# Performance work log

Hardware: AMD Instinct MI355X
Metric: run time of the kernel (lower is better)

The kernel has to match this reference:

```python
import jax, jax.numpy as jnp
import numpy as np

N, M, D = 8192, 8192, 1024

def setup_inputs() -> dict:
    key = jax.random.key(0)
    k1, k2 = jax.random.split(key)
    encoder_outputs = jax.random.normal(k1, (N, D), dtype=jnp.float32)
    fact_emb = jax.random.normal(k2, (M, D), dtype=jnp.float32)
    return {"encoder_outputs": encoder_outputs, "fact_emb": fact_emb}

def reference(encoder_outputs, fact_emb):
    # energy: [N, M] = encoder_outputs @ fact_emb^T (unscaled)
    energy = jnp.einsum('nd,md->nm', encoder_outputs, fact_emb)
    weights = jax.nn.softmax(energy, axis=1)          # softmax over facts
    outputs = jnp.einsum('nm,md->nd', weights, fact_emb)
    return (outputs, weights)
```

## Files before the change

kernel.cpp:

```cpp
#include <hip/hip_runtime.h>
#include <hip/hip_bf16.h>
#include <math.h>
#include <stdint.h>

#define N_ROWS 8192
#define M_FACTS 8192
#define D_DIM 1024

typedef __bf16 bf16x8_t __attribute__((ext_vector_type(8)));
typedef __bf16 bf16x4_t __attribute__((ext_vector_type(4)));
typedef float f32x4_t __attribute__((ext_vector_type(4)));

#define BM 128
#define BN 128
#define BK 32
#define PADK 40

__device__ __forceinline__ void gload_lds16(const void* g, void* lds) {
  __builtin_amdgcn_global_load_lds(
      (__attribute__((address_space(1))) void*)(uintptr_t)g,
      (__attribute__((address_space(3))) void*)(uint32_t)(uintptr_t)lds,
      16, 0, 0);
}

#define WAIT_VMCNT(n) __builtin_amdgcn_s_waitcnt(0x0F70 | (n))


__global__ __launch_bounds__(256) void split_hi_lo(const float* __restrict__ X,
                                                   __bf16* __restrict__ H,
                                                   __bf16* __restrict__ L) {
  int i = blockIdx.x * 256 + threadIdx.x;
  float4 v = ((const float4*)X)[i];
  float f[4] = {v.x, v.y, v.z, v.w};
  bf16x4_t h, l;
#pragma unroll
  for (int q = 0; q < 4; q++) {
    __bf16 hh = (__bf16)f[q];
    h[q] = hh;
    l[q] = (__bf16)(f[q] - (float)hh);
  }
  ((bf16x4_t*)H)[i] = h;
  ((bf16x4_t*)L)[i] = l;
}

__global__ __launch_bounds__(256) void transpose_f_bf16(const float* __restrict__ F,
                                                        __bf16* __restrict__ Ft) {
  __shared__ __bf16 t[64 * 68];
  const int tid = threadIdx.x;
  const int m0 = blockIdx.x * 64, d0 = blockIdx.y * 64;
#pragma unroll
  for (int p = 0; p < 4; p++) {
    int flat = p * 256 + tid;
    int m = flat >> 4, dq = flat & 15;
    float4 v = *(const float4*)(F + (size_t)(m0 + m) * D_DIM + d0 + dq * 4);
    bf16x4_t h;
    h[0] = (__bf16)v.x;
    h[1] = (__bf16)v.y;
    h[2] = (__bf16)v.z;
    h[3] = (__bf16)v.w;
    *(bf16x4_t*)(t + m * 68 + dq * 4) = h;
  }
  __syncthreads();
  int d = tid & 63, mc = (tid >> 6) * 16;
  bf16x8_t o0, o1;
#pragma unroll
  for (int j = 0; j < 8; j++) o0[j] = t[(mc + j) * 68 + d];
#pragma unroll
  for (int j = 0; j < 8; j++) o1[j] = t[(mc + 8 + j) * 68 + d];
  __bf16* dst = Ft + (size_t)(d0 + d) * M_FACTS + m0 + mc;
  *(bf16x8_t*)(dst) = o0;
  *(bf16x8_t*)(dst + 8) = o1;
}

__global__ __launch_bounds__(256) void gemm1_fast(const __bf16* __restrict__ Eh,
                                                  const __bf16* __restrict__ El,
                                                  const __bf16* __restrict__ Fh,
                                                  const __bf16* __restrict__ Fl,
                                                  float* __restrict__ C) {
  __shared__ __bf16 sAh[BM * BK], sAl[BM * BK], sBh[BN * BK], sBl[BN * BK];
  const int tid = threadIdx.x;
  const int wave = tid >> 6, lane = tid & 63;
  const int row0 = blockIdx.x * BM, col0 = blockIdx.y * BN;
  const int wm = wave >> 1, wn = wave & 1;
  const int lrow = lane & 15, quad = lane >> 4;

  f32x4_t acc[4][4];
#pragma unroll
  for (int i = 0; i < 4; i++)
#pragma unroll
    for (int j = 0; j < 4; j++) acc[i][j] = (f32x4_t){0.f, 0.f, 0.f, 0.f};

  for (int k0 = 0; k0 < D_DIM; k0 += BK) {
#pragma unroll
    for (int r = 0; r < 2; r++) {
      int c = (r * 4 + wave) * 64 + lane;
      int row = c >> 2;
      int ko = (c & 3) << 3;
      size_t ga = (size_t)(row0 + row) * D_DIM + k0 + ko;
      size_t gb = (size_t)(col0 + row) * D_DIM + k0 + ko;
      gload_lds16(Eh + ga, sAh + c * 8);
      gload_lds16(El + ga, sAl + c * 8);
      gload_lds16(Fh + gb, sBh + c * 8);
      gload_lds16(Fl + gb, sBl + c * 8);
    }
    __syncthreads();

    bf16x8_t ah[4], al[4], bh[4], bl[4];
#pragma unroll
    for (int i = 0; i < 4; i++) {
      int ra = (wm * 64 + i * 16 + lrow) * BK + quad * 8;
      ah[i] = *(const bf16x8_t*)(sAh + ra);
      al[i] = *(const bf16x8_t*)(sAl + ra);
      int rb = (wn * 64 + i * 16 + lrow) * BK + quad * 8;
      bh[i] = *(const bf16x8_t*)(sBh + rb);
      bl[i] = *(const bf16x8_t*)(sBl + rb);
    }
#pragma unroll
    for (int i = 0; i < 4; i++)
#pragma unroll
      for (int j = 0; j < 4; j++) {
        acc[i][j] = __builtin_amdgcn_mfma_f32_16x16x32_bf16(ah[i], bh[j], acc[i][j], 0, 0, 0);
        acc[i][j] = __builtin_amdgcn_mfma_f32_16x16x32_bf16(ah[i], bl[j], acc[i][j], 0, 0, 0);
        acc[i][j] = __builtin_amdgcn_mfma_f32_16x16x32_bf16(al[i], bh[j], acc[i][j], 0, 0, 0);
      }
    __syncthreads();
  }

#pragma unroll
  for (int i = 0; i < 4; i++) {
    int rbase = row0 + wm * 64 + i * 16 + quad * 4;
#pragma unroll
    for (int j = 0; j < 4; j++) {
      int c = col0 + wn * 64 + j * 16 + lrow;
#pragma unroll
      for (int r = 0; r < 4; r++) C[(size_t)(rbase + r) * M_FACTS + c] = acc[i][j][r];
    }
  }
}

#define G2BK 64
__global__ __launch_bounds__(256) void gemm2_db(const __bf16* __restrict__ Wb,
                                                const __bf16* __restrict__ Ft,
                                                float* __restrict__ O,
                                                int out_row0) {
  __shared__ __bf16 sW[2][BM * G2BK];
  __shared__ __bf16 sF[2][BN * G2BK];
  const int tid = threadIdx.x;
  const int wave = tid >> 6, lane = tid & 63;
  const int col0 = blockIdx.x * BN;
  const int row0 = blockIdx.y * BM;
  const int wm = wave >> 1, wn = wave & 1;
  const int lrow = lane & 15, quad = lane >> 4;

  const int lr = lane >> 3;
  const int lk = (lane & 7) * 8;

  f32x4_t acc[4][4];
#pragma unroll
  for (int i = 0; i < 4; i++)
#pragma unroll
    for (int j = 0; j < 4; j++) acc[i][j] = (f32x4_t){0.f, 0.f, 0.f, 0.f};

#pragma unroll
  for (int r = 0; r < 4; r++) {
    int c = wave * 4 + r;
    int row = c * 8 + lr;
    gload_lds16(Wb + (size_t)(row0 + row) * M_FACTS + 0 + lk, &sW[0][c * 512 + lane * 8]);
    gload_lds16(Ft + (size_t)(col0 + row) * M_FACTS + 0 + lk, &sF[0][c * 512 + lane * 8]);
  }

  int buf = 0;
  for (int k0 = 0; k0 < M_FACTS; k0 += G2BK) {
    const bool more = (k0 + G2BK) < M_FACTS;
    if (more) {
      int nb = buf ^ 1;
#pragma unroll
      for (int r = 0; r < 4; r++) {
        int c = wave * 4 + r;
        int row = c * 8 + lr;
        gload_lds16(Wb + (size_t)(row0 + row) * M_FACTS + (k0 + G2BK) + lk,
                    &sW[nb][c * 512 + lane * 8]);
        gload_lds16(Ft + (size_t)(col0 + row) * M_FACTS + (k0 + G2BK) + lk,
                    &sF[nb][c * 512 + lane * 8]);
      }
      WAIT_VMCNT(8);
    } else {
      WAIT_VMCNT(0);
    }
    __builtin_amdgcn_s_barrier();

#pragma unroll
    for (int ks = 0; ks < G2BK; ks += 32) {
      bf16x8_t a[4], b[4];
#pragma unroll
      for (int i = 0; i < 4; i++) {
        a[i] = *(const bf16x8_t*)(&sW[buf][(wm * 64 + i * 16 + lrow) * G2BK + ks + quad * 8]);
        b[i] = *(const bf16x8_t*)(&sF[buf][(wn * 64 + i * 16 + lrow) * G2BK + ks + quad * 8]);
      }
#pragma unroll
      for (int i = 0; i < 4; i++)
#pragma unroll
        for (int j = 0; j < 4; j++)
          acc[i][j] = __builtin_amdgcn_mfma_f32_16x16x32_bf16(a[i], b[j], acc[i][j], 0, 0, 0);
    }
    __builtin_amdgcn_s_barrier();
    buf ^= 1;
  }

#pragma unroll
  for (int i = 0; i < 4; i++) {
    int rbase = out_row0 + row0 + wm * 64 + i * 16 + quad * 4;
#pragma unroll
    for (int j = 0; j < 4; j++) {
      int c = col0 + wn * 64 + j * 16 + lrow;
#pragma unroll
      for (int r = 0; r < 4; r++) O[(size_t)(rbase + r) * D_DIM + c] = acc[i][j][r];
    }
  }
}

__global__ __launch_bounds__(256) void gemm2_mid(const float* __restrict__ W,
                                                 const __bf16* __restrict__ Ft,
                                                 float* __restrict__ O) {
  __shared__ __bf16 sW[BM * BK], sF[BN * BK];
  const int tid = threadIdx.x;
  const int wave = tid >> 6, lane = tid & 63;
  const int row0 = blockIdx.x * BM, col0 = blockIdx.y * BN;
  const int wm = wave >> 1, wn = wave & 1;
  const int lrow = lane & 15, quad = lane >> 4;

  f32x4_t acc[4][4];
#pragma unroll
  for (int i = 0; i < 4; i++)
#pragma unroll
    for (int j = 0; j < 4; j++) acc[i][j] = (f32x4_t){0.f, 0.f, 0.f, 0.f};

  for (int k0 = 0; k0 < M_FACTS; k0 += BK) {
#pragma unroll
    for (int r = 0; r < 2; r++) {
      int c = (r * 4 + wave) * 64 + lane;
      int row = c >> 2;
      int ko = (c & 3) << 3;
      gload_lds16(Ft + (size_t)(col0 + row) * M_FACTS + k0 + ko, sF + c * 8);
    }
#pragma unroll
    for (int it = 0; it < 4; it++) {
      int flat = it * 256 + tid;
      int r = flat >> 3, q = flat & 7;
      float4 v = *(const float4*)(W + (size_t)(row0 + r) * M_FACTS + k0 + q * 4);
      bf16x4_t h;
      h[0] = (__bf16)v.x;
      h[1] = (__bf16)v.y;
      h[2] = (__bf16)v.z;
      h[3] = (__bf16)v.w;
      *(bf16x4_t*)(sW + r * BK + q * 4) = h;
    }
    __syncthreads();

    bf16x8_t a[4], b[4];
#pragma unroll
    for (int i = 0; i < 4; i++) {
      a[i] = *(const bf16x8_t*)(sW + (wm * 64 + i * 16 + lrow) * BK + quad * 8);
      b[i] = *(const bf16x8_t*)(sF + (wn * 64 + i * 16 + lrow) * BK + quad * 8);
    }
#pragma unroll
    for (int i = 0; i < 4; i++)
#pragma unroll
      for (int j = 0; j < 4; j++)
        acc[i][j] = __builtin_amdgcn_mfma_f32_16x16x32_bf16(a[i], b[j], acc[i][j], 0, 0, 0);
    __syncthreads();
  }

#pragma unroll
  for (int i = 0; i < 4; i++) {
    int rbase = row0 + wm * 64 + i * 16 + quad * 4;
#pragma unroll
    for (int j = 0; j < 4; j++) {
      int c = col0 + wn * 64 + j * 16 + lrow;
#pragma unroll
      for (int r = 0; r < 4; r++) O[(size_t)(rbase + r) * D_DIM + c] = acc[i][j][r];
    }
  }
}

template <bool EMIT_BF16>
__global__ __launch_bounds__(256) void softmax_rows_t(float* __restrict__ W,
                                                      __bf16* __restrict__ Wb) {
  __shared__ float red[8];
  const int tid = threadIdx.x;
  float* p = W + (size_t)blockIdx.x * M_FACTS;

  float4 v[8];
  float mx = -3.4e38f;
#pragma unroll
  for (int i = 0; i < 8; i++) {
    v[i] = *(const float4*)(p + (size_t)(i * 256 + tid) * 4);
    mx = fmaxf(mx, fmaxf(fmaxf(v[i].x, v[i].y), fmaxf(v[i].z, v[i].w)));
  }
#pragma unroll
  for (int off = 32; off >= 1; off >>= 1) mx = fmaxf(mx, __shfl_xor(mx, off));
  const int wave = tid >> 6, lane = tid & 63;
  if (lane == 0) red[wave] = mx;
  __syncthreads();
  mx = fmaxf(fmaxf(red[0], red[1]), fmaxf(red[2], red[3]));

  float s = 0.f;
#pragma unroll
  for (int i = 0; i < 8; i++) {
    v[i].x = __expf(v[i].x - mx);
    v[i].y = __expf(v[i].y - mx);
    v[i].z = __expf(v[i].z - mx);
    v[i].w = __expf(v[i].w - mx);
    s += v[i].x + v[i].y + v[i].z + v[i].w;
  }
#pragma unroll
  for (int off = 32; off >= 1; off >>= 1) s += __shfl_xor(s, off);
  if (lane == 0) red[4 + wave] = s;
  __syncthreads();
  s = red[4] + red[5] + red[6] + red[7];
  float inv = 1.0f / s;
  __bf16* pb = EMIT_BF16 ? (Wb + (size_t)blockIdx.x * M_FACTS) : nullptr;
#pragma unroll
  for (int i = 0; i < 8; i++) {
    v[i].x *= inv;
    v[i].y *= inv;
    v[i].z *= inv;
    v[i].w *= inv;
    *(float4*)(p + (size_t)(i * 256 + tid) * 4) = v[i];
    if (EMIT_BF16) {
      bf16x4_t h;
      h[0] = (__bf16)v[i].x;
      h[1] = (__bf16)v[i].y;
      h[2] = (__bf16)v[i].z;
      h[3] = (__bf16)v[i].w;
      *(bf16x4_t*)(pb + (size_t)(i * 256 + tid) * 4) = h;
    }
  }
}

__global__ __launch_bounds__(256) void gemm1_energy(const float* __restrict__ A,
                                                    const float* __restrict__ B,
                                                    float* __restrict__ C) {
  __shared__ __align__(16) __bf16 sAh[BM * PADK];
  __shared__ __align__(16) __bf16 sAl[BM * PADK];
  __shared__ __align__(16) __bf16 sBh[BN * PADK];
  __shared__ __align__(16) __bf16 sBl[BN * PADK];

  const int tid = threadIdx.x;
  const int row0 = blockIdx.x * BM, col0 = blockIdx.y * BN;
  const int wave = tid >> 6, lane = tid & 63;
  const int wm = wave >> 1, wn = wave & 1;
  const int lrow = lane & 15, quad = lane >> 4;

  f32x4_t acc[4][4];
#pragma unroll
  for (int i = 0; i < 4; i++)
#pragma unroll
    for (int j = 0; j < 4; j++) acc[i][j] = (f32x4_t){0.f, 0.f, 0.f, 0.f};

  for (int k0 = 0; k0 < D_DIM; k0 += BK) {
    __syncthreads();
#pragma unroll
    for (int it = 0; it < 4; it++) {
      int flat = it * 256 + tid;
      int r = flat >> 3, kq = flat & 7;
      float4 va = *(const float4*)(A + (size_t)(row0 + r) * D_DIM + k0 + kq * 4);
      float4 vb = *(const float4*)(B + (size_t)(col0 + r) * D_DIM + k0 + kq * 4);
      float fa[4] = {va.x, va.y, va.z, va.w};
      float fb[4] = {vb.x, vb.y, vb.z, vb.w};
      bf16x4_t ah, al, bh, bl;
#pragma unroll
      for (int q = 0; q < 4; q++) {
        __bf16 h = (__bf16)fa[q];
        ah[q] = h;
        al[q] = (__bf16)(fa[q] - (float)h);
        __bf16 g = (__bf16)fb[q];
        bh[q] = g;
        bl[q] = (__bf16)(fb[q] - (float)g);
      }
      *(bf16x4_t*)(sAh + r * PADK + kq * 4) = ah;
      *(bf16x4_t*)(sAl + r * PADK + kq * 4) = al;
      *(bf16x4_t*)(sBh + r * PADK + kq * 4) = bh;
      *(bf16x4_t*)(sBl + r * PADK + kq * 4) = bl;
    }
    __syncthreads();

    bf16x8_t a_h[4], a_l[4], b_h[4], b_l[4];
#pragma unroll
    for (int i = 0; i < 4; i++) {
      int ra = wm * 64 + i * 16 + lrow;
      a_h[i] = *(const bf16x8_t*)(sAh + ra * PADK + quad * 8);
      a_l[i] = *(const bf16x8_t*)(sAl + ra * PADK + quad * 8);
      int rb = wn * 64 + i * 16 + lrow;
      b_h[i] = *(const bf16x8_t*)(sBh + rb * PADK + quad * 8);
      b_l[i] = *(const bf16x8_t*)(sBl + rb * PADK + quad * 8);
    }
#pragma unroll
    for (int i = 0; i < 4; i++)
#pragma unroll
      for (int j = 0; j < 4; j++) {
        acc[i][j] = __builtin_amdgcn_mfma_f32_16x16x32_bf16(a_h[i], b_h[j], acc[i][j], 0, 0, 0);
        acc[i][j] = __builtin_amdgcn_mfma_f32_16x16x32_bf16(a_h[i], b_l[j], acc[i][j], 0, 0, 0);
        acc[i][j] = __builtin_amdgcn_mfma_f32_16x16x32_bf16(a_l[i], b_h[j], acc[i][j], 0, 0, 0);
      }
  }

#pragma unroll
  for (int i = 0; i < 4; i++) {
    int rbase = row0 + wm * 64 + i * 16 + quad * 4;
#pragma unroll
    for (int j = 0; j < 4; j++) {
      int c = col0 + wn * 64 + j * 16 + lrow;
#pragma unroll
      for (int r = 0; r < 4; r++) C[(size_t)(rbase + r) * M_FACTS + c] = acc[i][j][r];
    }
  }
}

__global__ __launch_bounds__(256) void gemm2_out(const float* __restrict__ W,
                                                 const float* __restrict__ F,
                                                 float* __restrict__ O) {
  __shared__ __align__(16) __bf16 sW[BM * PADK];
  __shared__ __align__(16) __bf16 sFt[BN * PADK];

  const int tid = threadIdx.x;
  const int row0 = blockIdx.x * BM, col0 = blockIdx.y * BN;
  const int wave = tid >> 6, lane = tid & 63;
  const int wm = wave >> 1, wn = wave & 1;
  const int lrow = lane & 15, quad = lane >> 4;

  f32x4_t acc[4][4];
#pragma unroll
  for (int i = 0; i < 4; i++)
#pragma unroll
    for (int j = 0; j < 4; j++) acc[i][j] = (f32x4_t){0.f, 0.f, 0.f, 0.f};

  for (int k0 = 0; k0 < M_FACTS; k0 += BK) {
    __syncthreads();
#pragma unroll
    for (int it = 0; it < 4; it++) {
      int flat = it * 256 + tid;
      int r = flat >> 3, kq = flat & 7;
      float4 v = *(const float4*)(W + (size_t)(row0 + r) * M_FACTS + k0 + kq * 4);
      bf16x4_t h;
      h[0] = (__bf16)v.x;
      h[1] = (__bf16)v.y;
      h[2] = (__bf16)v.z;
      h[3] = (__bf16)v.w;
      *(bf16x4_t*)(sW + r * PADK + kq * 4) = h;
    }
#pragma unroll
    for (int it = 0; it < 4; it++) {
      int flat = it * 256 + tid;
      int m = flat >> 5, dq = flat & 31;
      float4 v = *(const float4*)(F + (size_t)(k0 + m) * D_DIM + col0 + dq * 4);
      sFt[(dq * 4 + 0) * PADK + m] = (__bf16)v.x;
      sFt[(dq * 4 + 1) * PADK + m] = (__bf16)v.y;
      sFt[(dq * 4 + 2) * PADK + m] = (__bf16)v.z;
      sFt[(dq * 4 + 3) * PADK + m] = (__bf16)v.w;
    }
    __syncthreads();

    bf16x8_t a[4], b[4];
#pragma unroll
    for (int i = 0; i < 4; i++) {
      a[i] = *(const bf16x8_t*)(sW + (wm * 64 + i * 16 + lrow) * PADK + quad * 8);
      b[i] = *(const bf16x8_t*)(sFt + (wn * 64 + i * 16 + lrow) * PADK + quad * 8);
    }
#pragma unroll
    for (int i = 0; i < 4; i++)
#pragma unroll
      for (int j = 0; j < 4; j++)
        acc[i][j] = __builtin_amdgcn_mfma_f32_16x16x32_bf16(a[i], b[j], acc[i][j], 0, 0, 0);
  }

#pragma unroll
  for (int i = 0; i < 4; i++) {
    int rbase = row0 + wm * 64 + i * 16 + quad * 4;
#pragma unroll
    for (int j = 0; j < 4; j++) {
      int c = col0 + wn * 64 + j * 16 + lrow;
#pragma unroll
      for (int r = 0; r < 4; r++) O[(size_t)(rbase + r) * D_DIM + c] = acc[i][j][r];
    }
  }
}

extern "C" void kernel_launch(void* const* d_in, const int* in_sizes, int n_in,
                              void* d_out, int out_size, void* d_ws, size_t ws_size,
                              hipStream_t stream) {
  const float* E = (const float*)d_in[0];
  const float* F = (const float*)d_in[1];
  float* outputs = (float*)d_out;
  float* weights = (float*)d_out + (size_t)N_ROWS * D_DIM;

  const size_t MB = 1ull << 20;
  char* ws = (char*)d_ws;

  const bool t1 = ws_size >= 144 * MB;
  const bool t2 = !t1 && ws_size >= 80 * MB;
  const bool hasFtOnly = !t1 && !t2 && ws_size >= 16 * MB;

  if (t1 || t2) {
    __bf16* Ft = (__bf16*)(ws + 0 * MB);
    __bf16* Eh = (__bf16*)(ws + 16 * MB);
    __bf16* El = (__bf16*)(ws + 32 * MB);
    __bf16* Fh = (__bf16*)(ws + 48 * MB);
    __bf16* Fl = (__bf16*)(ws + 64 * MB);
    __bf16* Wb = (__bf16*)(ws + 16 * MB);

    transpose_f_bf16<<<dim3(M_FACTS / 64, D_DIM / 64), 256, 0, stream>>>(F, Ft);
    split_hi_lo<<<dim3((N_ROWS * D_DIM) / 1024), 256, 0, stream>>>(E, Eh, El);
    split_hi_lo<<<dim3((M_FACTS * D_DIM) / 1024), 256, 0, stream>>>(F, Fh, Fl);
    gemm1_fast<<<dim3(N_ROWS / BM, M_FACTS / BN), 256, 0, stream>>>(Eh, El, Fh, Fl, weights);

    if (t1) {
      softmax_rows_t<true><<<dim3(N_ROWS), 256, 0, stream>>>(weights, Wb);
      gemm2_db<<<dim3(D_DIM / BN, N_ROWS / BM), 256, 0, stream>>>(Wb, Ft, outputs, 0);
    } else {
      const int HALF = N_ROWS / 2;
      for (int h = 0; h < 2; h++) {
        float* Wchunk = weights + (size_t)h * HALF * M_FACTS;
        softmax_rows_t<true><<<dim3(HALF), 256, 0, stream>>>(Wchunk, Wb);
        gemm2_db<<<dim3(D_DIM / BN, HALF / BM), 256, 0, stream>>>(Wb, Ft, outputs, h * HALF);
      }
    }
  } else {
    __bf16* Ft = (__bf16*)ws;
    if (hasFtOnly) {
      transpose_f_bf16<<<dim3(M_FACTS / 64, D_DIM / 64), 256, 0, stream>>>(F, Ft);
    }
    gemm1_energy<<<dim3(N_ROWS / BM, M_FACTS / BN), 256, 0, stream>>>(E, F, weights);
    softmax_rows_t<false><<<dim3(N_ROWS), 256, 0, stream>>>(weights, nullptr);
    if (hasFtOnly) {
      gemm2_mid<<<dim3(N_ROWS / BM, D_DIM / BN), 256, 0, stream>>>(weights, Ft, outputs);
    } else {
      gemm2_out<<<dim3(N_ROWS / BM, D_DIM / BN), 256, 0, stream>>>(weights, F, outputs);
    }
  }
}
```

Baseline: 998.8 us.

## Register-staged gemm2 pipeline, chunked gemm1 launches, fp32 LDS transpose

Replaces the async global-to-LDS double-buffered gemm2 with a version that prefetches the next K tile into registers and then writes it into a double-buffered LDS tile, using a smaller K step. gemm1 is split into eight launches over row bands, presumably for better L2 reuse of the F operand. The transpose kernel now stages fp32 values transposed in LDS and converts to bf16 on the way out. The aim is better latency hiding and cache locality, at the cost of more launches and extra register and LDS store traffic.

```diff
diff --git a/kernel.cpp b/kernel.cpp
--- a/kernel.cpp
+++ b/kernel.cpp
@@ -22,8 +22,6 @@
       (__attribute__((address_space(3))) void*)(uint32_t)(uintptr_t)lds,
       16, 0, 0);
 }
-
-#define WAIT_VMCNT(n) __builtin_amdgcn_s_waitcnt(0x0F70 | (n))
 
 
 __global__ __launch_bounds__(256) void split_hi_lo(const float* __restrict__ X,
@@ -45,7 +43,7 @@
 
 __global__ __launch_bounds__(256) void transpose_f_bf16(const float* __restrict__ F,
                                                         __bf16* __restrict__ Ft) {
-  __shared__ __bf16 t[64 * 68];
+  __shared__ float t[64 * 69];
   const int tid = threadIdx.x;
   const int m0 = blockIdx.x * 64, d0 = blockIdx.y * 64;
 #pragma unroll
@@ -53,34 +51,34 @@
     int flat = p * 256 + tid;
     int m = flat >> 4, dq = flat & 15;
     float4 v = *(const float4*)(F + (size_t)(m0 + m) * D_DIM + d0 + dq * 4);
-    bf16x4_t h;
-    h[0] = (__bf16)v.x;
-    h[1] = (__bf16)v.y;
-    h[2] = (__bf16)v.z;
-    h[3] = (__bf16)v.w;
-    *(bf16x4_t*)(t + m * 68 + dq * 4) = h;
+    t[(dq * 4 + 0) * 69 + m] = v.x;
+    t[(dq * 4 + 1) * 69 + m] = v.y;
+    t[(dq * 4 + 2) * 69 + m] = v.z;
+    t[(dq * 4 + 3) * 69 + m] = v.w;
   }
   __syncthreads();
-  int d = tid & 63, mc = (tid >> 6) * 16;
-  bf16x8_t o0, o1;
-#pragma unroll
-  for (int j = 0; j < 8; j++) o0[j] = t[(mc + j) * 68 + d];
-#pragma unroll
-  for (int j = 0; j < 8; j++) o1[j] = t[(mc + 8 + j) * 68 + d];
-  __bf16* dst = Ft + (size_t)(d0 + d) * M_FACTS + m0 + mc;
-  *(bf16x8_t*)(dst) = o0;
-  *(bf16x8_t*)(dst + 8) = o1;
+#pragma unroll
+  for (int q = 0; q < 2; q++) {
+    int id = q * 256 + tid;
+    int d = id >> 3, c = id & 7;
+    const float* row = t + d * 69 + c * 8;
+    bf16x8_t o;
+#pragma unroll
+    for (int i = 0; i < 8; i++) o[i] = (__bf16)row[i];
+    *(bf16x8_t*)(Ft + (size_t)(d0 + d) * M_FACTS + m0 + c * 8) = o;
+  }
 }
 
 __global__ __launch_bounds__(256) void gemm1_fast(const __bf16* __restrict__ Eh,
                                                   const __bf16* __restrict__ El,
                                                   const __bf16* __restrict__ Fh,
                                                   const __bf16* __restrict__ Fl,
-                                                  float* __restrict__ C) {
+                                                  float* __restrict__ C,
+                                                  int row_base) {
   __shared__ __bf16 sAh[BM * BK], sAl[BM * BK], sBh[BN * BK], sBl[BN * BK];
   const int tid = threadIdx.x;
   const int wave = tid >> 6, lane = tid & 63;
-  const int row0 = blockIdx.x * BM, col0 = blockIdx.y * BN;
+  const int row0 = row_base + blockIdx.x * BM, col0 = blockIdx.y * BN;
   const int wm = wave >> 1, wn = wave & 1;
   const int lrow = lane & 15, quad = lane >> 4;
 
@@ -138,13 +136,12 @@
   }
 }
 
-#define G2BK 64
-__global__ __launch_bounds__(256) void gemm2_db(const __bf16* __restrict__ Wb,
-                                                const __bf16* __restrict__ Ft,
-                                                float* __restrict__ O,
-                                                int out_row0) {
-  __shared__ __bf16 sW[2][BM * G2BK];
-  __shared__ __bf16 sF[2][BN * G2BK];
+__global__ __launch_bounds__(256) void gemm2_reg(const __bf16* __restrict__ Wb,
+                                                 const __bf16* __restrict__ Ft,
+                                                 float* __restrict__ O,
+                                                 int out_row0) {
+  __shared__ __bf16 sW[2][BM * BK];
+  __shared__ __bf16 sF[2][BN * BK];
   const int tid = threadIdx.x;
   const int wave = tid >> 6, lane = tid & 63;
   const int col0 = blockIdx.x * BN;
@@ -152,8 +149,13 @@
   const int wm = wave >> 1, wn = wave & 1;
   const int lrow = lane & 15, quad = lane >> 4;
 
-  const int lr = lane >> 3;
-  const int lk = (lane & 7) * 8;
+  const int id0 = wave * 64 + lane;
+  const int r0 = id0 >> 2, c0 = (id0 & 3) << 3;
+  const int id1 = id0 + 256;
+  const int r1 = id1 >> 2, c1 = (id1 & 3) << 3;
+
+  const __bf16* gW = Wb + (size_t)row0 * M_FACTS;
+  const __bf16* gF = Ft + (size_t)col0 * M_FACTS;
 
   f32x4_t acc[4][4];
 #pragma unroll
@@ -161,50 +163,52 @@
 #pragma unroll
     for (int j = 0; j < 4; j++) acc[i][j] = (f32x4_t){0.f, 0.f, 0.f, 0.f};
 
-#pragma unroll
-  for (int r = 0; r < 4; r++) {
-    int c = wave * 4 + r;
-    int row = c * 8 + lr;
-    gload_lds16(Wb + (size_t)(row0 + row) * M_FACTS + 0 + lk, &sW[0][c * 512 + lane * 8]);
-    gload_lds16(Ft + (size_t)(col0 + row) * M_FACTS + 0 + lk, &sF[0][c * 512 + lane * 8]);
-  }
-
-  int buf = 0;
-  for (int k0 = 0; k0 < M_FACTS; k0 += G2BK) {
-    const bool more = (k0 + G2BK) < M_FACTS;
-    if (more) {
-      int nb = buf ^ 1;
-#pragma unroll
-      for (int r = 0; r < 4; r++) {
-        int c = wave * 4 + r;
-        int row = c * 8 + lr;
-        gload_lds16(Wb + (size_t)(row0 + row) * M_FACTS + (k0 + G2BK) + lk,
-                    &sW[nb][c * 512 + lane * 8]);
-        gload_lds16(Ft + (size_t)(col0 + row) * M_FACTS + (k0 + G2BK) + lk,
-                    &sF[nb][c * 512 + lane * 8]);
+  bf16x8_t rW0, rW1, rF0, rF1;
+  rW0 = *(const bf16x8_t*)(gW + (size_t)r0 * M_FACTS + c0);
+  rW1 = *(const bf16x8_t*)(gW + (size_t)r1 * M_FACTS + c1);
+  rF0 = *(const bf16x8_t*)(gF + (size_t)r0 * M_FACTS + c0);
+  rF1 = *(const bf16x8_t*)(gF + (size_t)r1 * M_FACTS + c1);
+  *(bf16x8_t*)(&sW[0][id0 * 8]) = rW0;
+  *(bf16x8_t*)(&sW[0][id1 * 8]) = rW1;
+  *(bf16x8_t*)(&sF[0][id0 * 8]) = rF0;
+  *(bf16x8_t*)(&sF[0][id1 * 8]) = rF1;
+  rW0 = *(const bf16x8_t*)(gW + (size_t)r0 * M_FACTS + BK + c0);
+  rW1 = *(const bf16x8_t*)(gW + (size_t)r1 * M_FACTS + BK + c1);
+  rF0 = *(const bf16x8_t*)(gF + (size_t)r0 * M_FACTS + BK + c0);
+  rF1 = *(const bf16x8_t*)(gF + (size_t)r1 * M_FACTS + BK + c1);
+  __syncthreads();
+
+  const int NT = M_FACTS / BK;
+  for (int it = 0; it < NT; it++) {
+    const int cur = it & 1;
+    bf16x8_t a[4], b[4];
+#pragma unroll
+    for (int i = 0; i < 4; i++) {
+      a[i] = *(const bf16x8_t*)(&sW[cur][(wm * 64 + i * 16 + lrow) * BK + quad * 8]);
+      b[i] = *(const bf16x8_t*)(&sF[cur][(wn * 64 + i * 16 + lrow) * BK + quad * 8]);
+    }
+#pragma unroll
+    for (int i = 0; i < 4; i++)
+#pragma unroll
+      for (int j = 0; j < 4; j++)
+        acc[i][j] = __builtin_amdgcn_mfma_f32_16x16x32_bf16(a[i], b[j], acc[i][j], 0, 0, 0);
+
+    __syncthreads();
+    if (it + 1 < NT) {
+      const int nxt = cur ^ 1;
+      *(bf16x8_t*)(&sW[nxt][id0 * 8]) = rW0;
+      *(bf16x8_t*)(&sW[nxt][id1 * 8]) = rW1;
+      *(bf16x8_t*)(&sF[nxt][id0 * 8]) = rF0;
+      *(bf16x8_t*)(&sF[nxt][id1 * 8]) = rF1;
+      if (it + 2 < NT) {
+        const int ko = (it + 2) * BK;
+        rW0 = *(const bf16x8_t*)(gW + (size_t)r0 * M_FACTS + ko + c0);
+        rW1 = *(const bf16x8_t*)(gW + (size_t)r1 * M_FACTS + ko + c1);
+        rF0 = *(const bf16x8_t*)(gF + (size_t)r0 * M_FACTS + ko + c0);
+        rF1 = *(const bf16x8_t*)(gF + (size_t)r1 * M_FACTS + ko + c1);
       }
-      WAIT_VMCNT(8);
-    } else {
-      WAIT_VMCNT(0);
-    }
-    __builtin_amdgcn_s_barrier();
-
-#pragma unroll
-    for (int ks = 0; ks < G2BK; ks += 32) {
-      bf16x8_t a[4], b[4];
-#pragma unroll
-      for (int i = 0; i < 4; i++) {
-        a[i] = *(const bf16x8_t*)(&sW[buf][(wm * 64 + i * 16 + lrow) * G2BK + ks + quad * 8]);
-        b[i] = *(const bf16x8_t*)(&sF[buf][(wn * 64 + i * 16 + lrow) * G2BK + ks + quad * 8]);
-      }
-#pragma unroll
-      for (int i = 0; i < 4; i++)
-#pragma unroll
-        for (int j = 0; j < 4; j++)
-          acc[i][j] = __builtin_amdgcn_mfma_f32_16x16x32_bf16(a[i], b[j], acc[i][j], 0, 0, 0);
-    }
-    __builtin_amdgcn_s_barrier();
-    buf ^= 1;
+      __syncthreads();
+    }
   }
 
 #pragma unroll
@@ -512,17 +516,20 @@
     transpose_f_bf16<<<dim3(M_FACTS / 64, D_DIM / 64), 256, 0, stream>>>(F, Ft);
     split_hi_lo<<<dim3((N_ROWS * D_DIM) / 1024), 256, 0, stream>>>(E, Eh, El);
     split_hi_lo<<<dim3((M_FACTS * D_DIM) / 1024), 256, 0, stream>>>(F, Fh, Fl);
-    gemm1_fast<<<dim3(N_ROWS / BM, M_FACTS / BN), 256, 0, stream>>>(Eh, El, Fh, Fl, weights);
+    for (int b = 0; b < 8; b++) {
+      gemm1_fast<<<dim3(8, M_FACTS / BN), 256, 0, stream>>>(Eh, El, Fh, Fl, weights,
+                                                            b * (N_ROWS / 8));
+    }
 
     if (t1) {
       softmax_rows_t<true><<<dim3(N_ROWS), 256, 0, stream>>>(weights, Wb);
-      gemm2_db<<<dim3(D_DIM / BN, N_ROWS / BM), 256, 0, stream>>>(Wb, Ft, outputs, 0);
+      gemm2_reg<<<dim3(D_DIM / BN, N_ROWS / BM), 256, 0, stream>>>(Wb, Ft, outputs, 0);
     } else {
       const int HALF = N_ROWS / 2;
       for (int h = 0; h < 2; h++) {
         float* Wchunk = weights + (size_t)h * HALF * M_FACTS;
         softmax_rows_t<true><<<dim3(HALF), 256, 0, stream>>>(Wchunk, Wb);
-        gemm2_db<<<dim3(D_DIM / BN, HALF / BM), 256, 0, stream>>>(Wb, Ft, outputs, h * HALF);
+        gemm2_reg<<<dim3(D_DIM / BN, HALF / BM), 256, 0, stream>>>(Wb, Ft, outputs, h * HALF);
       }
     }
   } else {
```

Result: slower. 1.084 ms (+8.5%).
